# Optimization experiments

Hardware: AMD Instinct MI355X
Metric: run time of the kernel (lower is better)

Reference implementation:

```python
import jax, jax.numpy as jnp
import numpy as np

B, T, D, F_FF, E, TOP_K = 8, 2048, 1024, 4096, 8, 2
CAP_FACTOR = 1.25


def setup_inputs() -> dict:
    key = jax.random.key(0)
    ks = jax.random.split(key, 7)
    s = 0.02
    return {
        "x": jax.random.normal(ks[0], (B, T, D), dtype=jnp.float32),
        "w_router": jax.random.normal(ks[1], (D, E), dtype=jnp.float32) * s,
        "b_router": jnp.zeros((E,), dtype=jnp.float32),
        "w1": jax.random.normal(ks[2], (E, D, F_FF), dtype=jnp.float32) * s,
        "b1": jnp.zeros((E, F_FF), dtype=jnp.float32),
        "w2": jax.random.normal(ks[3], (E, F_FF, D), dtype=jnp.float32) * s,
        "b2": jnp.zeros((E, D), dtype=jnp.float32),
    }


def reference(x, w_router, b_router, w1, b1, w2, b2):
    b, t, d = x.shape
    n = b * t
    e = w_router.shape[1]
    xf = x.reshape(n, d)

    # router in float32 (as original: .float())
    logits = xf.astype(jnp.float32) @ w_router + b_router
    gates = jax.nn.softmax(logits, axis=-1)              # [N, E]
    topv, topi = jax.lax.top_k(gates, TOP_K)             # [N, K]

    cap = max(1, int(CAP_FACTOR * n / e))

    # flatten assignments in (token, slot) order -> matches python loop order
    e_flat = topi.reshape(-1)                            # [N*K] expert id
    g_flat = topv.reshape(-1)                            # [N*K] gate value
    tok = jnp.repeat(jnp.arange(n), TOP_K)               # [N*K] token id

    # position of each assignment inside its expert (arrival order)
    onehot = jax.nn.one_hot(e_flat, e, dtype=jnp.int32)  # [N*K, E]
    pos = jnp.cumsum(onehot, axis=0)[jnp.arange(n * TOP_K), e_flat] - 1
    keep = pos < cap                                     # capacity dropping
    posc = jnp.minimum(pos, cap - 1)

    # dispatch: [E, cap, D] buffers (unique kept slots -> scatter-add safe)
    buf = jnp.zeros((e, cap, d), x.dtype).at[e_flat, posc].add(
        jnp.where(keep[:, None], xf[tok], 0.0))

    # per-expert FFN as grouped GEMM (exact GELU, as torch nn.GELU default)
    h = jax.nn.gelu(jnp.einsum('ecd,edf->ecf', buf, w1) + b1[:, None, :],
                    approximate=False)
    out = jnp.einsum('ecf,efd->ecd', h, w2) + b2[:, None, :]

    # combine: weighted scatter-add back to tokens
    og = out[e_flat, posc]                               # [N*K, D]
    w = jnp.where(keep, g_flat, 0.0).astype(x.dtype)
    y = jnp.zeros((n, d), x.dtype).at[tok].add(w[:, None] * og)
    ws = jnp.zeros((n,), x.dtype).at[tok].add(w)
    y = jnp.where((ws > 0.0)[:, None], y / jnp.maximum(ws, 1e-6)[:, None], y)
    return y.reshape(b, t, d)
```

## Files before the change

kernel.cpp:

```cpp
#include <hip/hip_runtime.h>

#define NTOK   16384
#define DMODEL 1024
#define FFF    4096
#define NEXP   8
#define CAP    2560
#define NASSIGN (NTOK*2)

typedef __bf16 bf16x8 __attribute__((ext_vector_type(8)));
typedef float  f32x4  __attribute__((ext_vector_type(4)));
typedef unsigned short u16x8 __attribute__((ext_vector_type(8)));

__device__ __forceinline__ unsigned short f2bf(float f) {
    unsigned int u = __float_as_uint(f);
    u = u + 0x7FFFu + ((u >> 16) & 1u);
    return (unsigned short)(u >> 16);
}
__device__ __forceinline__ float bf2f(unsigned short s) {
    return __uint_as_float(((unsigned int)s) << 16);
}

__global__ void router_kernel(const float* __restrict__ x,
                              const float* __restrict__ wr,
                              const float* __restrict__ br,
                              int* __restrict__ topi,
                              float* __restrict__ topv) {
    int t    = blockIdx.x * 4 + (threadIdx.x >> 6);
    int lane = threadIdx.x & 63;
    const float4* xr4 = reinterpret_cast<const float4*>(x + (size_t)t * DMODEL);
    float a[8] = {0.f,0.f,0.f,0.f,0.f,0.f,0.f,0.f};
    #pragma unroll
    for (int i = lane; i < DMODEL/4; i += 64) {
        float4 xv = xr4[i];
        const float* w = wr + i * 32;
        #pragma unroll
        for (int e = 0; e < 8; e++) a[e] = fmaf(xv.x, w[e],      a[e]);
        #pragma unroll
        for (int e = 0; e < 8; e++) a[e] = fmaf(xv.y, w[8 + e],  a[e]);
        #pragma unroll
        for (int e = 0; e < 8; e++) a[e] = fmaf(xv.z, w[16 + e], a[e]);
        #pragma unroll
        for (int e = 0; e < 8; e++) a[e] = fmaf(xv.w, w[24 + e], a[e]);
    }
    #pragma unroll
    for (int off = 32; off > 0; off >>= 1) {
        #pragma unroll
        for (int e = 0; e < 8; e++) a[e] += __shfl_xor(a[e], off, 64);
    }
    if (lane == 0) {
        float l[8], g[8];
        float mx = -1e30f;
        #pragma unroll
        for (int e = 0; e < 8; e++) { l[e] = a[e] + br[e]; mx = fmaxf(mx, l[e]); }
        float s = 0.f;
        #pragma unroll
        for (int e = 0; e < 8; e++) { g[e] = expf(l[e] - mx); s += g[e]; }
        float inv = 1.f / s;
        #pragma unroll
        for (int e = 0; e < 8; e++) g[e] *= inv;
        float v1 = -1.f, v2 = -1.f; int i1 = 0, i2 = 0;
        #pragma unroll
        for (int e = 0; e < 8; e++) {
            float v = g[e];
            if (v > v1)      { v2 = v1; i2 = i1; v1 = v; i1 = e; }
            else if (v > v2) { v2 = v; i2 = e; }
        }
        topi[t*2]   = i1; topi[t*2+1] = i2;
        topv[t*2]   = v1; topv[t*2+1] = v2;
    }
}

__global__ void scan_kernel(const int* __restrict__ topi,
                            int* __restrict__ pos,
                            int* __restrict__ slot_tok,
                            int* __restrict__ kept) {
    const int APT = NASSIGN / 256;
    int tid = threadIdx.x, lane = tid & 63, w = tid >> 6;
    int base = tid * APT;
    const int4* tp = reinterpret_cast<const int4*>(topi + base);
    int c[8] = {0,0,0,0,0,0,0,0};
    for (int i = 0; i < APT/4; i++) {
        int4 v = tp[i];
        #pragma unroll
        for (int q = 0; q < 8; q++)
            c[q] += (v.x == q) + (v.y == q) + (v.z == q) + (v.w == q);
    }
    int excl[8], wtot[8];
    #pragma unroll
    for (int e = 0; e < 8; e++) {
        int s = c[e];
        for (int off = 1; off < 64; off <<= 1) {
            int n = __shfl_up(s, off, 64);
            if (lane >= off) s += n;
        }
        excl[e] = s - c[e];
        wtot[e] = __shfl(s, 63, 64);
    }
    __shared__ int woff[4][8];
    if (lane == 0) {
        #pragma unroll
        for (int e = 0; e < 8; e++) woff[w][e] = wtot[e];
    }
    __syncthreads();
    if (tid == 0) {
        for (int e = 0; e < 8; e++) {
            int run = 0;
            for (int ww = 0; ww < 4; ww++) { int t0 = woff[ww][e]; woff[ww][e] = run; run += t0; }
            kept[e] = run < CAP ? run : CAP;
        }
    }
    __syncthreads();
    int run[8];
    #pragma unroll
    for (int e = 0; e < 8; e++) run[e] = woff[w][e] + excl[e];
    for (int i = 0; i < APT/4; i++) {
        int4 v = tp[i];
        int ev[4] = {v.x, v.y, v.z, v.w};
        #pragma unroll
        for (int u = 0; u < 4; u++) {
            int a = base + i*4 + u;
            int e = ev[u];
            int p = 0;
            #pragma unroll
            for (int q = 0; q < 8; q++) if (e == q) { p = run[q]; run[q] = p + 1; }
            pos[a] = p;
            if (p < CAP) slot_tok[(size_t)e * CAP + p] = a >> 1;
        }
    }
}

__global__ void dispatch_kernel(const float* __restrict__ x,
                                const int* __restrict__ slot_tok,
                                const int* __restrict__ kept,
                                unsigned short* __restrict__ xb) {
    int row  = blockIdx.x * 4 + (threadIdx.x >> 6);
    int lane = threadIdx.x & 63;
    int e = row / CAP;
    int p = row - e * CAP;
    if (p >= kept[e]) return;
    int t = slot_tok[row];
    const float4* src = reinterpret_cast<const float4*>(x + (size_t)t * DMODEL);
    ushort4* dst = reinterpret_cast<ushort4*>(xb + (size_t)row * DMODEL);
    #pragma unroll
    for (int i = lane; i < DMODEL/4; i += 64) {
        float4 v = src[i];
        ushort4 o;
        o.x = f2bf(v.x); o.y = f2bf(v.y); o.z = f2bf(v.z); o.w = f2bf(v.w);
        dst[i] = o;
    }
}

__global__ void transpose_f32_to_bf16(const float* __restrict__ in,
                                      unsigned short* __restrict__ out,
                                      int R, int C) {
    __shared__ float tile[64 * 65];
    int e = blockIdx.z;
    const float* src = in + (size_t)e * R * C;
    unsigned short* dst = out + (size_t)e * R * C;
    int c0 = blockIdx.x * 64, r0 = blockIdx.y * 64;
    int t = threadIdx.x;
    int lr4 = (t & 15) * 4;
    #pragma unroll
    for (int s = 0; s < 4; s++) {
        int r = (t >> 4) + s * 16;
        float4 v = *reinterpret_cast<const float4*>(&src[(size_t)(r0 + r) * C + c0 + lr4]);
        float* tr = &tile[r * 65 + lr4];
        tr[0] = v.x; tr[1] = v.y; tr[2] = v.z; tr[3] = v.w;
    }
    __syncthreads();
    int j = t & 7;
    int ccb = t >> 3;
    #pragma unroll
    for (int s = 0; s < 2; s++) {
        int cc = ccb + s * 32;
        u16x8 o;
        #pragma unroll
        for (int k = 0; k < 8; k++) o[k] = f2bf(tile[(j * 8 + k) * 65 + cc]);
        *reinterpret_cast<u16x8*>(&dst[(size_t)(c0 + cc) * R + r0 + j * 8]) = o;
    }
}

template<int GELU>
__global__ __launch_bounds__(256, 2)
void gemm_bt(const unsigned short* __restrict__ A,
             const unsigned short* __restrict__ Bt,
             const float* __restrict__ bias,
             unsigned short* __restrict__ C,
             int M, int N, int K) {
    constexpr int BM = 128, BN = 128, BK = 64;
    __shared__ unsigned short As[BM * 64];
    __shared__ unsigned short Bs[BN * 64];
    const int e = blockIdx.z;
    const unsigned short* Ab = A  + (size_t)e * M * K + (size_t)blockIdx.y * BM * K;
    const unsigned short* Bb = Bt + (size_t)e * N * K + (size_t)blockIdx.x * BN * K;
    const float* bp = bias + (size_t)e * N;
    const int tid  = threadIdx.x;
    const int lane = tid & 63;
    const int wv   = tid >> 6;
    const int wm   = (wv >> 1) * 64;
    const int wn   = (wv & 1) * 64;
    const int lr   = lane & 15;
    const int quad = lane >> 4;
    const int srow   = lane >> 3;
    const int schunk = (lane & 7) ^ srow;
    const int swiz   = lr & 7;

    f32x4 acc[4][4] = {};

    for (int kb = 0; kb < K; kb += BK) {
        #pragma unroll
        for (int s = 0; s < 4; s++) {
            int q = wv * 4 + s;
            int row = q * 8 + srow;
            __builtin_amdgcn_global_load_lds(
                (const __attribute__((address_space(1))) unsigned int*)(Ab + (size_t)row * K + kb + schunk * 8),
                (__attribute__((address_space(3))) unsigned int*)(As + q * 512),
                16, 0, 0);
            __builtin_amdgcn_global_load_lds(
                (const __attribute__((address_space(1))) unsigned int*)(Bb + (size_t)row * K + kb + schunk * 8),
                (__attribute__((address_space(3))) unsigned int*)(Bs + q * 512),
                16, 0, 0);
        }
        __syncthreads();
        #pragma unroll
        for (int kk = 0; kk < BK; kk += 32) {
            bf16x8 af[4], bfr[4];
            const int sc = ((kk >> 3) + quad) ^ swiz;
            #pragma unroll
            for (int i = 0; i < 4; i++)
                af[i] = *reinterpret_cast<const bf16x8*>(&As[(wm + i*16 + lr) * 64 + sc * 8]);
            #pragma unroll
            for (int j = 0; j < 4; j++)
                bfr[j] = *reinterpret_cast<const bf16x8*>(&Bs[(wn + j*16 + lr) * 64 + sc * 8]);
            #pragma unroll
            for (int i = 0; i < 4; i++)
                #pragma unroll
                for (int j = 0; j < 4; j++)
                    acc[i][j] = __builtin_amdgcn_mfma_f32_16x16x32_bf16(af[i], bfr[j], acc[i][j], 0, 0, 0);
        }
        __syncthreads();
    }

    size_t cbase = (size_t)e * M * N + (size_t)blockIdx.y * BM * N + (size_t)blockIdx.x * BN;
    float bv[4];
    #pragma unroll
    for (int j = 0; j < 4; j++) bv[j] = bp[blockIdx.x * BN + wn + j * 16 + lr];
    #pragma unroll
    for (int i = 0; i < 4; i++) {
        #pragma unroll
        for (int r = 0; r < 4; r++) {
            int row = wm + i * 16 + quad * 4 + r;
            #pragma unroll
            for (int j = 0; j < 4; j++) {
                int col = wn + j * 16 + lr;
                float v = acc[i][j][r] + bv[j];
                if (GELU) v = 0.5f * v * (1.f + erff(v * 0.70710678118654752440f));
                C[cbase + (size_t)row * N + col] = f2bf(v);
            }
        }
    }
}

__global__ void combine_kernel(const int* __restrict__ topi,
                               const float* __restrict__ topv,
                               const int* __restrict__ pos,
                               const unsigned short* __restrict__ out2,
                               float* __restrict__ y) {
    int t    = blockIdx.x * 4 + (threadIdx.x >> 6);
    int lane = threadIdx.x & 63;
    int e0 = topi[t*2],   e1 = topi[t*2+1];
    float g0 = topv[t*2], g1 = topv[t*2+1];
    int p0 = pos[t*2],    p1 = pos[t*2+1];
    float w0 = (p0 < CAP) ? g0 : 0.f;
    float w1 = (p1 < CAP) ? g1 : 0.f;
    float wsum = w0 + w1;
    float scale = (wsum > 0.f) ? 1.f / fmaxf(wsum, 1e-6f) : 0.f;
    int q0 = p0 < CAP ? p0 : CAP - 1;
    int q1 = p1 < CAP ? p1 : CAP - 1;
    const ushort4* o0 = reinterpret_cast<const ushort4*>(out2 + ((size_t)e0 * CAP + q0) * DMODEL);
    const ushort4* o1 = reinterpret_cast<const ushort4*>(out2 + ((size_t)e1 * CAP + q1) * DMODEL);
    float4* dst = reinterpret_cast<float4*>(y + (size_t)t * DMODEL);
    #pragma unroll
    for (int i = lane; i < DMODEL/4; i += 64) {
        ushort4 a = o0[i], b = o1[i];
        float4 r;
        r.x = (w0 * bf2f(a.x) + w1 * bf2f(b.x)) * scale;
        r.y = (w0 * bf2f(a.y) + w1 * bf2f(b.y)) * scale;
        r.z = (w0 * bf2f(a.z) + w1 * bf2f(b.z)) * scale;
        r.w = (w0 * bf2f(a.w) + w1 * bf2f(b.w)) * scale;
        dst[i] = r;
    }
}

extern "C" void kernel_launch(void* const* d_in, const int* in_sizes, int n_in,
                              void* d_out, int out_size, void* d_ws, size_t ws_size,
                              hipStream_t stream) {
    (void)in_sizes; (void)n_in; (void)out_size; (void)ws_size;
    const float* x        = (const float*)d_in[0];
    const float* w_router = (const float*)d_in[1];
    const float* b_router = (const float*)d_in[2];
    const float* w1       = (const float*)d_in[3];
    const float* b1       = (const float*)d_in[4];
    const float* w2       = (const float*)d_in[5];
    const float* b2       = (const float*)d_in[6];
    float* y = (float*)d_out;

    char* ws = (char*)d_ws;
    size_t off = 0;
    auto alloc = [&](size_t n) { char* p = ws + off; off = (off + n + 255) & ~(size_t)255; return p; };
    int*   topi     = (int*)  alloc((size_t)NASSIGN * 4);
    float* topv     = (float*)alloc((size_t)NASSIGN * 4);
    int*   pos      = (int*)  alloc((size_t)NASSIGN * 4);
    int*   slot_tok = (int*)  alloc((size_t)NEXP * CAP * 4);
    int*   kept     = (int*)  alloc(8 * 4);
    unsigned short* w1t = (unsigned short*)alloc((size_t)NEXP * DMODEL * FFF * 2);
    unsigned short* w2t = (unsigned short*)alloc((size_t)NEXP * DMODEL * FFF * 2);
    unsigned short* xb  = (unsigned short*)alloc((size_t)NEXP * CAP * DMODEL * 2);
    unsigned short* h   = (unsigned short*)alloc((size_t)NEXP * CAP * FFF * 2);
    unsigned short* out2 = w1t;

    router_kernel<<<NTOK/4, 256, 0, stream>>>(x, w_router, b_router, topi, topv);
    scan_kernel<<<1, 256, 0, stream>>>(topi, pos, slot_tok, kept);
    dispatch_kernel<<<NEXP*CAP/4, 256, 0, stream>>>(x, slot_tok, kept, xb);
    transpose_f32_to_bf16<<<dim3(FFF/64, DMODEL/64, NEXP), 256, 0, stream>>>(w1, w1t, DMODEL, FFF);
    transpose_f32_to_bf16<<<dim3(DMODEL/64, FFF/64, NEXP), 256, 0, stream>>>(w2, w2t, FFF, DMODEL);
    gemm_bt<1><<<dim3(FFF/128, CAP/128, NEXP), 256, 0, stream>>>(xb, w1t, b1, h, CAP, FFF, DMODEL);
    gemm_bt<0><<<dim3(DMODEL/128, CAP/128, NEXP), 256, 0, stream>>>(h, w2t, b2, out2, CAP, DMODEL, FFF);
    combine_kernel<<<NTOK/4, 256, 0, stream>>>(topi, topv, pos, out2, y);
}
```

Before: 914.6 us.

## Merge router and weight transposes into one prologue; swizzle GEMM block order

Router and both weight transpose/convert kernels now run as one launch, split by block index, so the small router work overlaps the bandwidth-heavy transposes and two launches go away. The GEMM grid is flattened and remapped so that consecutive blocks walk down M inside chunks of up to 8 N-tiles. This is meant to raise L2 reuse of the A and B tiles. The block-range split in the prologue is hardcoded, and every prologue block now reserves the transpose shared-memory tile, which may lower occupancy for the router blocks.

After: 913.1 us. About the same (-0.2%).

```diff
diff --git a/kernel.cpp b/kernel.cpp
--- a/kernel.cpp
+++ b/kernel.cpp
@@ -20,12 +20,12 @@
     return __uint_as_float(((unsigned int)s) << 16);
 }
 
-__global__ void router_kernel(const float* __restrict__ x,
-                              const float* __restrict__ wr,
-                              const float* __restrict__ br,
-                              int* __restrict__ topi,
-                              float* __restrict__ topv) {
-    int t    = blockIdx.x * 4 + (threadIdx.x >> 6);
+__device__ void router_body(int rb, const float* __restrict__ x,
+                            const float* __restrict__ wr,
+                            const float* __restrict__ br,
+                            int* __restrict__ topi,
+                            float* __restrict__ topv) {
+    int t    = rb * 4 + (threadIdx.x >> 6);
     int lane = threadIdx.x & 63;
     const float4* xr4 = reinterpret_cast<const float4*>(x + (size_t)t * DMODEL);
     float a[8] = {0.f,0.f,0.f,0.f,0.f,0.f,0.f,0.f};
@@ -67,6 +67,61 @@
         }
         topi[t*2]   = i1; topi[t*2+1] = i2;
         topv[t*2]   = v1; topv[t*2+1] = v2;
+    }
+}
+
+__device__ void transpose_body(const float* __restrict__ src,
+                               unsigned short* __restrict__ dst,
+                               int R, int C, int r0, int c0) {
+    __shared__ float tile[64 * 65];
+    int t = threadIdx.x;
+    int lr4 = (t & 15) * 4;
+    #pragma unroll
+    for (int s = 0; s < 4; s++) {
+        int r = (t >> 4) + s * 16;
+        float4 v = *reinterpret_cast<const float4*>(&src[(size_t)(r0 + r) * C + c0 + lr4]);
+        float* tr = &tile[r * 65 + lr4];
+        tr[0] = v.x; tr[1] = v.y; tr[2] = v.z; tr[3] = v.w;
+    }
+    __syncthreads();
+    int j = t & 7;
+    int ccb = t >> 3;
+    #pragma unroll
+    for (int s = 0; s < 2; s++) {
+        int cc = ccb + s * 32;
+        u16x8 o;
+        #pragma unroll
+        for (int k = 0; k < 8; k++) o[k] = f2bf(tile[(j * 8 + k) * 65 + cc]);
+        *reinterpret_cast<u16x8*>(&dst[(size_t)(c0 + cc) * R + r0 + j * 8]) = o;
+    }
+}
+
+__global__ void prologue_kernel(const float* __restrict__ x,
+                                const float* __restrict__ wr,
+                                const float* __restrict__ br,
+                                const float* __restrict__ w1,
+                                const float* __restrict__ w2,
+                                int* __restrict__ topi,
+                                float* __restrict__ topv,
+                                unsigned short* __restrict__ w1t,
+                                unsigned short* __restrict__ w2t) {
+    int id = blockIdx.x;
+    if (id < NTOK/4) {
+        router_body(id, x, wr, br, topi, topv);
+    } else if (id < NTOK/4 + 8192) {
+        int q = id - NTOK/4;
+        int e = q >> 10, t = q & 1023;
+        int bx = t & 63, by = t >> 6;
+        transpose_body(w1 + (size_t)e * DMODEL * FFF,
+                       w1t + (size_t)e * DMODEL * FFF,
+                       DMODEL, FFF, by * 64, bx * 64);
+    } else {
+        int q = id - NTOK/4 - 8192;
+        int e = q >> 10, t = q & 1023;
+        int bx = t & 15, by = t >> 4;
+        transpose_body(w2 + (size_t)e * DMODEL * FFF,
+                       w2t + (size_t)e * DMODEL * FFF,
+                       FFF, DMODEL, by * 64, bx * 64);
     }
 }
 
@@ -150,36 +205,6 @@
     }
 }
 
-__global__ void transpose_f32_to_bf16(const float* __restrict__ in,
-                                      unsigned short* __restrict__ out,
-                                      int R, int C) {
-    __shared__ float tile[64 * 65];
-    int e = blockIdx.z;
-    const float* src = in + (size_t)e * R * C;
-    unsigned short* dst = out + (size_t)e * R * C;
-    int c0 = blockIdx.x * 64, r0 = blockIdx.y * 64;
-    int t = threadIdx.x;
-    int lr4 = (t & 15) * 4;
-    #pragma unroll
-    for (int s = 0; s < 4; s++) {
-        int r = (t >> 4) + s * 16;
-        float4 v = *reinterpret_cast<const float4*>(&src[(size_t)(r0 + r) * C + c0 + lr4]);
-        float* tr = &tile[r * 65 + lr4];
-        tr[0] = v.x; tr[1] = v.y; tr[2] = v.z; tr[3] = v.w;
-    }
-    __syncthreads();
-    int j = t & 7;
-    int ccb = t >> 3;
-    #pragma unroll
-    for (int s = 0; s < 2; s++) {
-        int cc = ccb + s * 32;
-        u16x8 o;
-        #pragma unroll
-        for (int k = 0; k < 8; k++) o[k] = f2bf(tile[(j * 8 + k) * 65 + cc]);
-        *reinterpret_cast<u16x8*>(&dst[(size_t)(c0 + cc) * R + r0 + j * 8]) = o;
-    }
-}
-
 template<int GELU>
 __global__ __launch_bounds__(256, 2)
 void gemm_bt(const unsigned short* __restrict__ A,
@@ -191,8 +216,17 @@
     __shared__ unsigned short As[BM * 64];
     __shared__ unsigned short Bs[BN * 64];
     const int e = blockIdx.z;
-    const unsigned short* Ab = A  + (size_t)e * M * K + (size_t)blockIdx.y * BM * K;
-    const unsigned short* Bb = Bt + (size_t)e * N * K + (size_t)blockIdx.x * BN * K;
+    const int gx = N / BN, gy = M / BM;
+    const int nc = gx < 8 ? gx : 8;
+    int id = blockIdx.x;
+    const int per_chunk = nc * gy;
+    const int chunk = id / per_chunk;
+    const int r = id - chunk * per_chunk;
+    const int bn = chunk * nc + (r % nc);
+    const int bm = r / nc;
+
+    const unsigned short* Ab = A  + (size_t)e * M * K + (size_t)bm * BM * K;
+    const unsigned short* Bb = Bt + (size_t)e * N * K + (size_t)bn * BN * K;
     const float* bp = bias + (size_t)e * N;
     const int tid  = threadIdx.x;
     const int lane = tid & 63;
@@ -241,19 +275,19 @@
         __syncthreads();
     }
 
-    size_t cbase = (size_t)e * M * N + (size_t)blockIdx.y * BM * N + (size_t)blockIdx.x * BN;
+    size_t cbase = (size_t)e * M * N + (size_t)bm * BM * N + (size_t)bn * BN;
     float bv[4];
     #pragma unroll
-    for (int j = 0; j < 4; j++) bv[j] = bp[blockIdx.x * BN + wn + j * 16 + lr];
+    for (int j = 0; j < 4; j++) bv[j] = bp[bn * BN + wn + j * 16 + lr];
     #pragma unroll
     for (int i = 0; i < 4; i++) {
         #pragma unroll
-        for (int r = 0; r < 4; r++) {
-            int row = wm + i * 16 + quad * 4 + r;
+        for (int rr = 0; rr < 4; rr++) {
+            int row = wm + i * 16 + quad * 4 + rr;
             #pragma unroll
             for (int j = 0; j < 4; j++) {
                 int col = wn + j * 16 + lr;
-                float v = acc[i][j][r] + bv[j];
+                float v = acc[i][j][rr] + bv[j];
                 if (GELU) v = 0.5f * v * (1.f + erff(v * 0.70710678118654752440f));
                 C[cbase + (size_t)row * N + col] = f2bf(v);
             }
@@ -319,12 +353,11 @@
     unsigned short* h   = (unsigned short*)alloc((size_t)NEXP * CAP * FFF * 2);
     unsigned short* out2 = w1t;
 
-    router_kernel<<<NTOK/4, 256, 0, stream>>>(x, w_router, b_router, topi, topv);
+    prologue_kernel<<<NTOK/4 + 16384, 256, 0, stream>>>(
+        x, w_router, b_router, w1, w2, topi, topv, w1t, w2t);
     scan_kernel<<<1, 256, 0, stream>>>(topi, pos, slot_tok, kept);
     dispatch_kernel<<<NEXP*CAP/4, 256, 0, stream>>>(x, slot_tok, kept, xb);
-    transpose_f32_to_bf16<<<dim3(FFF/64, DMODEL/64, NEXP), 256, 0, stream>>>(w1, w1t, DMODEL, FFF);
-    transpose_f32_to_bf16<<<dim3(DMODEL/64, FFF/64, NEXP), 256, 0, stream>>>(w2, w2t, FFF, DMODEL);
-    gemm_bt<1><<<dim3(FFF/128, CAP/128, NEXP), 256, 0, stream>>>(xb, w1t, b1, h, CAP, FFF, DMODEL);
-    gemm_bt<0><<<dim3(DMODEL/128, CAP/128, NEXP), 256, 0, stream>>>(h, w2t, b2, out2, CAP, DMODEL, FFF);
+    gemm_bt<1><<<dim3((FFF/128)*(CAP/128), 1, NEXP), 256, 0, stream>>>(xb, w1t, b1, h, CAP, FFF, DMODEL);
+    gemm_bt<0><<<dim3((DMODEL/128)*(CAP/128), 1, NEXP), 256, 0, stream>>>(h, w2t, b2, out2, CAP, DMODEL, FFF);
     combine_kernel<<<NTOK/4, 256, 0, stream>>>(topi, topv, pos, out2, y);
 }
```
